# Optimization experiments

Measured on AMD Instinct MI355X. Metric: run time of the kernel, lower is better.

## Reference

```python
import jax, jax.numpy as jnp
import numpy as np

N_NODES = 10000
N_EDGES = 160000
N_FEAT = 128      # n_features
N_BASIS = 20      # n_basis
N_LAYERS = 3      # n_interactions
N_GRAPHS = 64
CUTOFF = 5.0
VOCAB = 119       # 118 elements + padding idx 0


def setup_inputs() -> dict:
    key = jax.random.key(0)
    ks = jax.random.split(key, 20)
    z = jax.random.randint(ks[0], (N_NODES,), 0, VOCAB)
    pos = jax.random.normal(ks[1], (N_NODES, 3), dtype=jnp.float32) * 2.0
    cell = jax.random.normal(ks[2], (N_GRAPHS, 3, 3), dtype=jnp.float32)
    batch = jnp.sort(jax.random.randint(ks[3], (N_NODES,), 0, N_GRAPHS))
    edge_index = jax.random.randint(ks[4], (2, N_EDGES), 0, N_NODES)

    s = 1.0 / np.sqrt(N_FEAT)
    node_emb = jax.random.normal(ks[5], (VOCAB, N_FEAT), dtype=jnp.float32) * 0.1
    node_emb = node_emb.at[0].set(0.0)  # padding_idx=0
    # per-layer stacked parameters (L, ...)
    mnp_W1 = jax.random.normal(ks[6], (N_LAYERS, N_FEAT, N_FEAT), dtype=jnp.float32) * s
    mnp_b1 = jnp.zeros((N_LAYERS, N_FEAT), dtype=jnp.float32)
    mnp_W2 = jax.random.normal(ks[7], (N_LAYERS, N_FEAT, N_FEAT), dtype=jnp.float32) * s
    mnp_b2 = jnp.zeros((N_LAYERS, N_FEAT), dtype=jnp.float32)
    me_W = jax.random.normal(ks[8], (N_LAYERS, N_BASIS, N_FEAT), dtype=jnp.float32) * (1.0 / np.sqrt(N_BASIS))
    em1_W1 = jax.random.normal(ks[9], (N_LAYERS, N_FEAT, N_FEAT), dtype=jnp.float32) * s
    em1_W2 = jax.random.normal(ks[10], (N_LAYERS, N_FEAT, N_FEAT), dtype=jnp.float32) * s
    em2_W1 = jax.random.normal(ks[11], (N_LAYERS, N_FEAT, N_FEAT), dtype=jnp.float32) * s
    em2_W2 = jax.random.normal(ks[12], (N_LAYERS, N_FEAT, N_FEAT), dtype=jnp.float32) * s
    eu_W = jax.random.normal(ks[13], (N_LAYERS, N_FEAT, N_FEAT), dtype=jnp.float32) * s
    return {
        "z": z, "pos": pos, "cell": cell, "batch": batch, "edge_index": edge_index,
        "node_emb": node_emb,
        "mnp_W1": mnp_W1, "mnp_b1": mnp_b1, "mnp_W2": mnp_W2, "mnp_b2": mnp_b2,
        "me_W": me_W, "em1_W1": em1_W1, "em1_W2": em1_W2,
        "em2_W1": em2_W1, "em2_W2": em2_W2, "eu_W": eu_W,
    }


def _edge_embedding(pos_d, edge_index):
    """Gaussian RBF x cosine cutoff; dir = unit displacement vectors."""
    i, j = edge_index[0], edge_index[1]
    diff = pos_d[j] - pos_d[i]                      # (E, 3)
    d = jnp.sqrt(jnp.sum(diff * diff, axis=-1) + 1e-12)  # (E,)
    dir_edge = diff / d[:, None]                    # (E, 3)
    centers = jnp.linspace(0.0, CUTOFF, N_BASIS)
    width = CUTOFF / N_BASIS
    rbf = jnp.exp(-jnp.square((d[:, None] - centers) / width))  # (E, B)
    fc = 0.5 * (jnp.cos(jnp.pi * d / CUTOFF) + 1.0) * (d < CUTOFF)
    return rbf * fc[:, None], dir_edge


def reference(z, pos, cell, batch, edge_index, node_emb,
              mnp_W1, mnp_b1, mnp_W2, mnp_b2, me_W,
              em1_W1, em1_W2, em2_W1, em2_W2, eu_W):
    n = z.shape[0]
    atom = node_emb[z]                                   # (N, F)
    force = jnp.zeros((n, 3, N_FEAT), dtype=pos.dtype)   # (N, 3, F)

    # strain displacement bookkeeping (identity in plain forward)
    disp = jnp.broadcast_to(jnp.eye(3, dtype=pos.dtype), cell.shape)  # (G,3,3)
    sym = 0.5 * (disp + jnp.swapaxes(disp, -1, -2))
    pos_d = jnp.einsum('nd,nde->ne', pos, sym[batch])

    dist_edge, dir_edge = _edge_embedding(pos_d, edge_index)
    i, j = edge_index[0], edge_index[1]

    for l in range(N_LAYERS):
        # invariant node/edge message parts
        h = jax.nn.silu(atom @ mnp_W1[l] + mnp_b1[l]) @ mnp_W2[l] + mnp_b2[l]  # (N,F)
        me = dist_edge @ me_W[l]                                               # (E,F)
        msg = me * h[i] * h[j]                                                 # (E,F)
        atom = atom + jax.ops.segment_sum(msg, i, num_segments=n)
        # equivariant messages
        e1 = (jax.nn.silu(msg @ em1_W1[l]) @ em1_W2[l])[:, None, :] * dir_edge[:, :, None]  # (E,3,F)
        e2 = (jax.nn.silu(msg @ em2_W1[l]) @ em2_W2[l])[:, None, :] * force[j]              # (E,3,F)
        force = force + jax.ops.segment_sum(e1 + e2, i, num_segments=n)
        atom = atom + jnp.sum(force * (force @ eu_W[l]), axis=1)
    return atom, force
```

## Files before the change

### kernel.cpp

```cpp
#include <hip/hip_runtime.h>
#include <hip/hip_bf16.h>
#include <math.h>

#define NN 10000
#define NE 160000
#define NF 128
#define NB 20
#define CUT 5.0f
#define TPS 136
#define TPF 132

typedef __attribute__((ext_vector_type(8))) short short8;
typedef __attribute__((ext_vector_type(4))) float floatx4;
typedef unsigned short u16;
typedef unsigned int u32;

__device__ __forceinline__ u16 f2b(float x){
  union { __hip_bfloat16 b; u16 u; } cv;
  cv.b = __float2bfloat16(x);
  return cv.u;
}
__device__ __forceinline__ float lo_bf(u32 w){ return __uint_as_float(w << 16); }
__device__ __forceinline__ float hi_bf(u32 w){ return __uint_as_float(w & 0xFFFF0000u); }
__device__ __forceinline__ float fast_silu(float v){
  return v * __builtin_amdgcn_rcpf(1.f + __expf(-v));
}
__device__ __forceinline__ float rdf(const void* p, size_t i, int isb){
  return isb ? __bfloat162float(((const __hip_bfloat16*)p)[i]) : ((const float*)p)[i];
}

__global__ __launch_bounds__(256) void k_detect(const void* __restrict__ w, int nelem,
                                                int* __restrict__ flag){
  __shared__ int cnt;
  if (threadIdx.x == 0) cnt = 0;
  __syncthreads();
  const u16* hw = (const u16*)w;
  int local = 0;
  for (int k = threadIdx.x; k < nelem; k += 256){
    u16 h = hw[k];
    int e = (h >> 7) & 0xFF;
    if ((h & 0x7FFF) == 0 || (e >= 103 && e <= 130)) local++;
  }
  atomicAdd(&cnt, local);
  __syncthreads();
  if (threadIdx.x == 0) *flag = (cnt >= (nelem * 9) / 10) ? 1 : 0;
}

struct PrepArgs {
  const void* csrc[4]; float* cdst[4]; int cn[4];
  const void* ssrc[7]; u16* sdst[7];
  const void* mesrc;   u16* medst;
};
__global__ __launch_bounds__(256) void k_prep(PrepArgs a, const int* __restrict__ flag){
  int y = blockIdx.y;
  int isb = *flag;
  if (y < 4){
    const void* s = a.csrc[y]; float* d = a.cdst[y]; int n = a.cn[y];
    for (int i = blockIdx.x*256 + threadIdx.x; i < n; i += gridDim.x*256)
      d[i] = rdf(s, i, isb);
  } else if (y < 11){
    const void* s = a.ssrc[y-4]; u16* d = a.sdst[y-4];
    int idx = blockIdx.x*256 + threadIdx.x;
    int l = idx >> 14, rem = idx & 16383;
    int j = rem & 7, lane = (rem >> 3) & 63, tn = (rem >> 9) & 7, tk = rem >> 12;
    int k = tk*32 + ((lane >> 4) & 3)*8 + j, n = tn*16 + (lane & 15);
    d[idx] = f2b(rdf(s, (size_t)l*16384 + k*NF + n, isb));
  } else {
    int idx = blockIdx.x*256 + threadIdx.x;
    if (idx >= 3*4096) return;
    int l = idx >> 12, rem = idx & 4095;
    int j = rem & 7, lane = (rem >> 3) & 63, tn = rem >> 9;
    int k = ((lane >> 4) & 3)*8 + j, n = tn*16 + (lane & 15);
    a.medst[idx] = (k < NB) ? f2b(rdf(a.mesrc, (size_t)l*NB*NF + k*NF + n, isb)) : (u16)0;
  }
}

__global__ __launch_bounds__(256) void k_hist(const int* __restrict__ ei, int* __restrict__ count){
  int e = blockIdx.x*256 + threadIdx.x;
  if (e < NE) atomicAdd(&count[ei[e]], 1);
}
__global__ __launch_bounds__(256) void k_scan(const int* __restrict__ count,
                                              int* __restrict__ rowptr, int* __restrict__ cursor){
  __shared__ int part[256];
  const int CH = (NN + 255) / 256;
  int t = threadIdx.x;
  int base = t * CH;
  int s = 0;
  for (int k = 0; k < CH; k++){ int i = base + k; if (i < NN) s += count[i]; }
  part[t] = s;
  __syncthreads();
  for (int off = 1; off < 256; off <<= 1){
    int v = (t >= off) ? part[t - off] : 0;
    __syncthreads();
    part[t] += v;
    __syncthreads();
  }
  int run = (t == 0) ? 0 : part[t - 1];
  for (int k = 0; k < CH; k++){
    int i = base + k;
    if (i < NN){ rowptr[i] = run; cursor[i] = run; run += count[i]; }
  }
  if (t == 255) rowptr[NN] = run;
}
__global__ __launch_bounds__(256) void k_scatter_embed(const int* __restrict__ ei,
                                                       int* __restrict__ cursor,
                                                       const float* __restrict__ pos,
                                                       int* __restrict__ iis, int* __restrict__ jjs,
                                                       float* __restrict__ ds,
                                                       float* __restrict__ dirs){
  int e = blockIdx.x * 256 + threadIdx.x;
  if (e >= NE) return;
  int i = ei[e], j = ei[NE + e];
  float dx = pos[j*3+0] - pos[i*3+0];
  float dy = pos[j*3+1] - pos[i*3+1];
  float dz = pos[j*3+2] - pos[i*3+2];
  float d = sqrtf(dx*dx + dy*dy + dz*dz + 1e-12f);
  float inv = 1.0f / d;
  int s = atomicAdd(&cursor[i], 1);
  iis[s] = i; jjs[s] = j;
  ds[s] = d;
  dirs[s*3+0] = dx*inv; dirs[s*3+1] = dy*inv; dirs[s*3+2] = dz*inv;
}
__global__ __launch_bounds__(256) void k_rbf(const float* __restrict__ ds,
                                             u16* __restrict__ rbfb){
  int e = blockIdx.x * 256 + threadIdx.x;
  if (e >= NE) return;
  float d = ds[e];
  float fc = (d < CUT) ? 0.5f*(cosf((float)M_PI*d*(1.0f/CUT)) + 1.0f) : 0.0f;
  u32 row[16];
  #pragma unroll
  for (int kk = 0; kk < 16; kk++){
    int k0 = kk*2, k1 = kk*2 + 1;
    u32 w = 0;
    if (k0 < NB){
      float t0 = (d - CUT*(float)k0/(float)(NB-1)) * ((float)NB/CUT);
      w = (u32)f2b(__expf(-t0*t0) * fc);
    }
    if (k1 < NB){
      float t1 = (d - CUT*(float)k1/(float)(NB-1)) * ((float)NB/CUT);
      w |= ((u32)f2b(__expf(-t1*t1) * fc)) << 16;
    }
    row[kk] = w;
  }
  float4* dst = (float4*)(rbfb + (size_t)e*32);
  #pragma unroll
  for (int jv = 0; jv < 4; jv++)
    dst[jv] = *(const float4*)&row[jv*4];
}

__global__ __launch_bounds__(128, 2) void k_mlp0(
    const int* __restrict__ z, const float* __restrict__ emb,
    float* __restrict__ atom,
    const u16* __restrict__ w1sw, const float* __restrict__ b1,
    const u16* __restrict__ w2sw, const float* __restrict__ b2,
    u32* __restrict__ hb)
{
  __shared__ __align__(16) u16 tileT[16][TPS];
  const int wv = threadIdx.x >> 6;
  const int lane = threadIdx.x & 63;
  const int q = lane >> 4, ln = lane & 15;
  const int n0 = blockIdx.x * 16;
  const int zn = z[n0 + ln];

  floatx4 c1[4];
  #pragma unroll
  for (int t = 0; t < 4; t++) c1[t] = (floatx4){0,0,0,0};
  #pragma unroll
  for (int tk = 0; tk < 4; tk++){
    const float4 u0 = *(const float4*)&emb[(size_t)zn*NF + tk*32 + q*8];
    const float4 u1 = *(const float4*)&emb[(size_t)zn*NF + tk*32 + q*8 + 4];
    if ((tk >> 1) == wv){
      *(float4*)&atom[(size_t)(n0+ln)*NF + tk*32 + q*8]     = u0;
      *(float4*)&atom[(size_t)(n0+ln)*NF + tk*32 + q*8 + 4] = u1;
    }
    short8 a;
    a[0]=(short)f2b(u0.x); a[1]=(short)f2b(u0.y); a[2]=(short)f2b(u0.z); a[3]=(short)f2b(u0.w);
    a[4]=(short)f2b(u1.x); a[5]=(short)f2b(u1.y); a[6]=(short)f2b(u1.z); a[7]=(short)f2b(u1.w);
    #pragma unroll
    for (int t = 0; t < 4; t++){
      short8 b = *(const short8*)(w1sw + (size_t)((tk*8 + wv*4 + t)*64 + lane)*8);
      c1[t] = __builtin_amdgcn_mfma_f32_16x16x32_bf16(a, b, c1[t], 0, 0, 0);
    }
  }
  #pragma unroll
  for (int t = 0; t < 4; t++){
    int n = (wv*4 + t)*16 + ln;
    float bias = b1[n];
    #pragma unroll
    for (int r = 0; r < 4; r++)
      tileT[q*4 + r][n] = f2b(fast_silu(c1[t][r] + bias));
  }
  __syncthreads();
  floatx4 c2[4];
  #pragma unroll
  for (int t = 0; t < 4; t++) c2[t] = (floatx4){0,0,0,0};
  #pragma unroll
  for (int tk = 0; tk < 4; tk++){
    short8 a = *(const short8*)&tileT[ln][tk*32 + q*8];
    #pragma unroll
    for (int t = 0; t < 4; t++){
      short8 b = *(const short8*)(w2sw + (size_t)((tk*8 + wv*4 + t)*64 + lane)*8);
      c2[t] = __builtin_amdgcn_mfma_f32_16x16x32_bf16(a, b, c2[t], 0, 0, 0);
    }
  }
  #pragma unroll
  for (int t = 0; t < 4; t++){
    float bias = b2[(wv*4 + t)*16 + ln];
    #pragma unroll
    for (int r = 0; r < 4; r++)
      ((u16*)hb)[(((size_t)(n0 + q*4 + r))*64 + t*16 + ln)*2 + wv] = f2b(c2[t][r] + bias);
  }
}

#define SEGFLUSH(ADDR_EXPR)                                               \
  {                                                                       \
    float s_ = 0.f;                                                       \
    _Pragma("unroll")                                                     \
    for (int m_ = 0; m_ < 16; m_++){                                      \
      s_ += tileF[m_][cc];                                                \
      if (m_ == 15 || ((bmask >> (m_ + 1)) & 1u)){                        \
        int ii_ = __builtin_amdgcn_readlane(curii, m_);                   \
        float* p_ = (ADDR_EXPR);                                          \
        atomicAdd(p_ + cc, s_);                                           \
        s_ = 0.f;                                                         \
      }                                                                   \
    }                                                                     \
  }

__global__ __launch_bounds__(128, 4) void k_edge_mfma(
    const int* __restrict__ iis, const int* __restrict__ jjs,
    const u16* __restrict__ rbfb, const float* __restrict__ dirs,
    const u32* __restrict__ hb,
    const u16* __restrict__ mesw,
    const u16* __restrict__ w11sw, const u16* __restrict__ w12sw,
    const u16* __restrict__ w21sw, const u16* __restrict__ w22sw,
    float* __restrict__ atom, const u32* __restrict__ forceb, float* __restrict__ force)
{
  __shared__ __align__(16) u16 tileM[16][TPS];
  __shared__ __align__(16) float tileF[16][TPF];
  u16* tileFu = (u16*)&tileF[0][0];

  const int wv = threadIdx.x >> 6;
  const int lane = threadIdx.x & 63;
  const int q = lane >> 4, ln = lane & 15;
  const int bid = (blockIdx.x & 7) * (gridDim.x >> 3) + (blockIdx.x >> 3);
  const int e0 = bid * 16;
  const int cc = wv*64 + lane;

  const int l16 = lane & 15;
  int curii = iis[e0 + l16];
  int previi = (l16 == 0) ? ~curii : iis[e0 + l16 - 1];
  const u32 bmask = (u32)__ballot(lane < 16 && (curii != previi));

  int iiR[4], jjR[4];
  float dirR[4][3];
  #pragma unroll
  for (int r = 0; r < 4; r++){
    int s = e0 + q*4 + r;
    iiR[r] = iis[s]; jjR[r] = jjs[s];
    dirR[r][0] = dirs[s*3+0]; dirR[r][1] = dirs[s*3+1]; dirR[r][2] = dirs[s*3+2];
  }

  u32 hiw[4][4], hjw[4][4];
  #pragma unroll
  for (int r = 0; r < 4; r++)
    #pragma unroll
    for (int t = 0; t < 4; t++){
      hiw[r][t] = hb[(size_t)iiR[r]*64 + t*16 + ln];
      hjw[r][t] = hb[(size_t)jjR[r]*64 + t*16 + ln];
    }

  short8 a_rbf = *(const short8*)(rbfb + (size_t)(e0 + ln)*32 + q*8);

  #pragma unroll
  for (int t = 0; t < 4; t++){
    const int tn_g = wv*4 + t;
    short8 b = *(const short8*)(mesw + (size_t)(tn_g*64 + lane)*8);
    floatx4 c = {0.f,0.f,0.f,0.f};
    c = __builtin_amdgcn_mfma_f32_16x16x32_bf16(a_rbf, b, c, 0, 0, 0);
    const int n = tn_g*16 + ln;
    #pragma unroll
    for (int r = 0; r < 4; r++){
      float hi_ = wv ? hi_bf(hiw[r][t]) : lo_bf(hiw[r][t]);
      float hj_ = wv ? hi_bf(hjw[r][t]) : lo_bf(hjw[r][t]);
      float mv = c[r] * hi_ * hj_;
      tileF[q*4 + r][n] = mv;
      tileM[q*4 + r][n] = f2b(mv);
    }
  }

  SEGFLUSH(&atom[(size_t)ii_ * NF])

  __syncthreads();

  floatx4 c2[4], c1[4];
  #pragma unroll
  for (int t = 0; t < 4; t++){ c2[t] = (floatx4){0,0,0,0}; c1[t] = (floatx4){0,0,0,0}; }
  #pragma unroll
  for (int tk = 0; tk < 4; tk++){
    short8 a = *(const short8*)&tileM[ln][tk*32 + q*8];
    #pragma unroll
    for (int t = 0; t < 4; t++){
      const int tn_g = wv*4 + t;
      short8 b2 = *(const short8*)(w21sw + (size_t)((tk*8 + tn_g)*64 + lane)*8);
      c2[t] = __builtin_amdgcn_mfma_f32_16x16x32_bf16(a, b2, c2[t], 0, 0, 0);
      short8 b1 = *(const short8*)(w11sw + (size_t)((tk*8 + tn_g)*64 + lane)*8);
      c1[t] = __builtin_amdgcn_mfma_f32_16x16x32_bf16(a, b1, c1[t], 0, 0, 0);
    }
  }
  #pragma unroll
  for (int t = 0; t < 4; t++){
    const int n = (wv*4 + t)*16 + ln;
    #pragma unroll
    for (int r = 0; r < 4; r++){
      tileFu[(q*4 + r)*TPS + n] = f2b(fast_silu(c1[t][r]));
      c2[t][r] = fast_silu(c2[t][r]);
    }
  }

  __syncthreads();

  floatx4 g1[4];
  #pragma unroll
  for (int t = 0; t < 4; t++) g1[t] = (floatx4){0,0,0,0};
  #pragma unroll
  for (int tk = 0; tk < 4; tk++){
    short8 a = *(const short8*)&tileFu[(size_t)ln*TPS + tk*32 + q*8];
    #pragma unroll
    for (int t = 0; t < 4; t++){
      short8 b = *(const short8*)(w12sw + (size_t)((tk*8 + wv*4 + t)*64 + lane)*8);
      g1[t] = __builtin_amdgcn_mfma_f32_16x16x32_bf16(a, b, g1[t], 0, 0, 0);
    }
  }
  #pragma unroll
  for (int t = 0; t < 4; t++){
    const int n = (wv*4 + t)*16 + ln;
    #pragma unroll
    for (int r = 0; r < 4; r++) tileM[q*4 + r][n] = f2b(c2[t][r]);
  }

  __syncthreads();

  floatx4 g2[4];
  #pragma unroll
  for (int t = 0; t < 4; t++) g2[t] = (floatx4){0,0,0,0};
  #pragma unroll
  for (int tk = 0; tk < 4; tk++){
    short8 a = *(const short8*)&tileM[ln][tk*32 + q*8];
    #pragma unroll
    for (int t = 0; t < 4; t++){
      short8 b = *(const short8*)(w22sw + (size_t)((tk*8 + wv*4 + t)*64 + lane)*8);
      g2[t] = __builtin_amdgcn_mfma_f32_16x16x32_bf16(a, b, g2[t], 0, 0, 0);
    }
  }

  for (int d = 0; d < 3; d++){
    u32 fjw[4][4];
    #pragma unroll
    for (int r = 0; r < 4; r++)
      #pragma unroll
      for (int t = 0; t < 4; t++)
        fjw[r][t] = forceb[((size_t)jjR[r]*3 + d)*64 + t*16 + ln];
    #pragma unroll
    for (int t = 0; t < 4; t++){
      const int n = (wv*4 + t)*16 + ln;
      #pragma unroll
      for (int r = 0; r < 4; r++){
        float fj = wv ? hi_bf(fjw[r][t]) : lo_bf(fjw[r][t]);
        tileF[q*4 + r][n] = g1[t][r]*dirR[r][d] + g2[t][r]*fj;
      }
    }
    SEGFLUSH(&force[((size_t)ii_*3 + d)*NF])
  }
}

__global__ __launch_bounds__(256, 2) void k_node(
    const float* __restrict__ force,
    const u16* __restrict__ eusw, u32* __restrict__ forceb,
    float* __restrict__ atom,
    const u16* __restrict__ w1sw, const float* __restrict__ b1,
    const u16* __restrict__ w2sw, const float* __restrict__ b2,
    u32* __restrict__ hb, int do_mlp)
{
  __shared__ __align__(16) u16 tileM3[3][16][TPS];
  __shared__ __align__(16) float tileF3[3][16][TPF];
  const int w = threadIdx.x >> 6;
  const int lane = threadIdx.x & 63;
  const int q = lane >> 4, ln = lane & 15;
  const int n0 = blockIdx.x * 16;
  const int cc2 = threadIdx.x & 127;
  const int mh  = (threadIdx.x >> 7) * 8;

  #pragma unroll
  for (int d = 0; d < 3; d++)
    #pragma unroll
    for (int m8 = 0; m8 < 8; m8++){
      int m = mh + m8;
      size_t idx = ((size_t)(n0+m)*3 + d)*NF + cc2;
      float v = force[idx];
      if (do_mlp)
        ((u16*)forceb)[(((size_t)(n0+m)*3 + d)*64 + (cc2 & 63))*2 + (cc2 >> 6)] = f2b(v);
      tileM3[d][m][cc2] = f2b(v);
      tileF3[d][m][cc2] = v;
    }
  __syncthreads();

  float acc[2][4];
  #pragma unroll
  for (int t = 0; t < 2; t++)
    #pragma unroll
    for (int r = 0; r < 4; r++) acc[t][r] = 0.f;

  #pragma unroll
  for (int d = 0; d < 3; d++){
    floatx4 c[2];
    #pragma unroll
    for (int t = 0; t < 2; t++) c[t] = (floatx4){0,0,0,0};
    #pragma unroll
    for (int tk = 0; tk < 4; tk++){
      short8 a = *(const short8*)&tileM3[d][ln][tk*32 + q*8];
      #pragma unroll
      for (int t = 0; t < 2; t++){
        short8 b = *(const short8*)(eusw + (size_t)((tk*8 + w*2 + t)*64 + lane)*8);
        c[t] = __builtin_amdgcn_mfma_f32_16x16x32_bf16(a, b, c[t], 0, 0, 0);
      }
    }
    #pragma unroll
    for (int t = 0; t < 2; t++){
      int n = (w*2 + t)*16 + ln;
      #pragma unroll
      for (int r = 0; r < 4; r++)
        acc[t][r] += tileF3[d][q*4 + r][n] * c[t][r];
    }
  }

  float anew[2][4];
  #pragma unroll
  for (int t = 0; t < 2; t++){
    int n = (w*2 + t)*16 + ln;
    #pragma unroll
    for (int r = 0; r < 4; r++){
      size_t idx = (size_t)(n0 + q*4 + r)*NF + n;
      float v = atom[idx] + acc[t][r];
      atom[idx] = v;
      anew[t][r] = v;
    }
  }
  if (!do_mlp) return;

  u16 (*tile)[TPS] = tileM3[0];
  __syncthreads();
  #pragma unroll
  for (int t = 0; t < 2; t++){
    int n = (w*2 + t)*16 + ln;
    #pragma unroll
    for (int r = 0; r < 4; r++) tile[q*4 + r][n] = f2b(anew[t][r]);
  }
  __syncthreads();
  floatx4 c1[2];
  #pragma unroll
  for (int t = 0; t < 2; t++) c1[t] = (floatx4){0,0,0,0};
  #pragma unroll
  for (int tk = 0; tk < 4; tk++){
    short8 a = *(const short8*)&tile[ln][tk*32 + q*8];
    #pragma unroll
    for (int t = 0; t < 2; t++){
      short8 b = *(const short8*)(w1sw + (size_t)((tk*8 + w*2 + t)*64 + lane)*8);
      c1[t] = __builtin_amdgcn_mfma_f32_16x16x32_bf16(a, b, c1[t], 0, 0, 0);
    }
  }
  __syncthreads();
  #pragma unroll
  for (int t = 0; t < 2; t++){
    int n = (w*2 + t)*16 + ln;
    float bias = b1[n];
    #pragma unroll
    for (int r = 0; r < 4; r++)
      tile[q*4 + r][n] = f2b(fast_silu(c1[t][r] + bias));
  }
  __syncthreads();
  floatx4 c2[2];
  #pragma unroll
  for (int t = 0; t < 2; t++) c2[t] = (floatx4){0,0,0,0};
  #pragma unroll
  for (int tk = 0; tk < 4; tk++){
    short8 a = *(const short8*)&tile[ln][tk*32 + q*8];
    #pragma unroll
    for (int t = 0; t < 2; t++){
      short8 b = *(const short8*)(w2sw + (size_t)((tk*8 + w*2 + t)*64 + lane)*8);
      c2[t] = __builtin_amdgcn_mfma_f32_16x16x32_bf16(a, b, c2[t], 0, 0, 0);
    }
  }
  #pragma unroll
  for (int t = 0; t < 2; t++){
    int tn = w*2 + t;
    float bias = b2[tn*16 + ln];
    #pragma unroll
    for (int r = 0; r < 4; r++)
      ((u16*)hb)[(((size_t)(n0 + q*4 + r))*64 + (tn & 3)*16 + ln)*2 + (tn >> 2)] = f2b(c2[t][r] + bias);
  }
}

__global__ __launch_bounds__(256) void k_writeout(const float* __restrict__ atom,
                                                  const float* __restrict__ force,
                                                  void* __restrict__ out,
                                                  const int* __restrict__ flag){
  int idx = blockIdx.x * 256 + threadIdx.x;
  const int na = NN * NF;
  const int tot = na + NN * 3 * NF;
  if (idx >= tot) return;
  float v = (idx < na) ? atom[idx] : force[idx - na];
  if (*flag) ((__hip_bfloat16*)out)[idx] = __float2bfloat16(v);
  else       ((float*)out)[idx] = v;
}

extern "C" void kernel_launch(void* const* d_in, const int* in_sizes, int n_in,
                              void* d_out, int out_size, void* d_ws, size_t ws_size,
                              hipStream_t stream){
  const int* z    = (const int*)d_in[0];
  const void* pos = d_in[1];
  const int* ei   = (const int*)d_in[4];
  const void* emb   = d_in[5];
  const void* mnpW1 = d_in[6];
  const void* mnpb1 = d_in[7];
  const void* mnpW2 = d_in[8];
  const void* mnpb2 = d_in[9];
  const void* meW   = d_in[10];
  const void* em1W1 = d_in[11];
  const void* em1W2 = d_in[12];
  const void* em2W1 = d_in[13];
  const void* em2W2 = d_in[14];
  const void* euW   = d_in[15];

  float* base  = (float*)d_ws;
  int*   flag  = (int*)d_ws;
  float* atom   = base + 4;
  float* force  = atom   + NN*NF;
  u32*   forceb = (u32*)(force + (size_t)NN*3*NF);
  int*   count  = (int*)(forceb + (size_t)NN*3*64);
  float* ds    = (float*)(count + NN);
  float* dirs  = ds + NE;
  float* posf  = dirs + 3*NE;
  float* embf  = posf + NN*3;
  float* b1f   = embf + 119*NF;
  float* b2f_  = b1f + 3*NF;
  u32*   hb    = (u32*)(b2f_ + 3*NF);
  u16*   mesw  = (u16*)(hb + (size_t)NN*64);
  u16*   w11sw = mesw  + 3*4096;
  u16*   w12sw = w11sw + 3*16384;
  u16*   w21sw = w12sw + 3*16384;
  u16*   w22sw = w21sw + 3*16384;
  u16*   w1sw  = w22sw + 3*16384;
  u16*   w2sw  = w1sw  + 3*16384;
  u16*   eusw  = w2sw  + 3*16384;
  int* rowptr  = (int*)(eusw + 3*16384);
  int* cursor  = rowptr + NN + 1;
  int* iis     = cursor + NN;
  int* jjs     = iis + NE;
  u16* rbfb    = (u16*)(jjs + NE);

  k_detect<<<1, 256, 0, stream>>>(meW, 3*NB*NF, flag);

  hipMemsetAsync(force, 0, ((size_t)NN*3*NF + (size_t)NN*3*64 + NN)*4, stream);

  PrepArgs pa;
  pa.csrc[0]=pos;   pa.cdst[0]=posf; pa.cn[0]=NN*3;
  pa.csrc[1]=emb;   pa.cdst[1]=embf; pa.cn[1]=119*NF;
  pa.csrc[2]=mnpb1; pa.cdst[2]=b1f;  pa.cn[2]=3*NF;
  pa.csrc[3]=mnpb2; pa.cdst[3]=b2f_; pa.cn[3]=3*NF;
  pa.ssrc[0]=em1W1; pa.sdst[0]=w11sw;
  pa.ssrc[1]=em1W2; pa.sdst[1]=w12sw;
  pa.ssrc[2]=em2W1; pa.sdst[2]=w21sw;
  pa.ssrc[3]=em2W2; pa.sdst[3]=w22sw;
  pa.ssrc[4]=mnpW1; pa.sdst[4]=w1sw;
  pa.ssrc[5]=mnpW2; pa.sdst[5]=w2sw;
  pa.ssrc[6]=euW;   pa.sdst[6]=eusw;
  pa.mesrc=meW;     pa.medst=mesw;
  k_prep<<<dim3(192,12), 256, 0, stream>>>(pa, flag);

  k_hist         <<<(NE+255)/256, 256, 0, stream>>>(ei, count);
  k_scan         <<<1, 256, 0, stream>>>(count, rowptr, cursor);
  k_scatter_embed<<<(NE+255)/256, 256, 0, stream>>>(ei, cursor, posf, iis, jjs, ds, dirs);
  k_rbf          <<<(NE+255)/256, 256, 0, stream>>>(ds, rbfb);

  k_mlp0<<<NN/16, 128, 0, stream>>>(z, embf, atom, w1sw, b1f, w2sw, b2f_, hb);
  for (int l = 0; l < 3; l++){
    k_edge_mfma<<<NE/16, 128, 0, stream>>>(iis, jjs, rbfb, dirs, hb,
        mesw  + (size_t)l*4096,
        w11sw + (size_t)l*16384, w12sw + (size_t)l*16384,
        w21sw + (size_t)l*16384, w22sw + (size_t)l*16384,
        atom, forceb, force);
    int nl = l + 1;
    k_node<<<NN/16, 256, 0, stream>>>(force,
        eusw + (size_t)l*16384, forceb, atom,
        w1sw + (size_t)(nl%3)*16384, b1f + (size_t)(nl%3)*NF,
        w2sw + (size_t)(nl%3)*16384, b2f_ + (size_t)(nl%3)*NF,
        hb, (l < 2) ? 1 : 0);
  }

  k_writeout<<<(NN*NF + NN*3*NF + 255)/256, 256, 0, stream>>>(atom, force, d_out, flag);
}
```

Measured before the change: 484.3 us.

## Split edge kernel column tiles across four waves per block

The edge kernel now launches 256 threads per block, so each of four waves handles two 16-column output tiles instead of four. Accumulator and gathered-feature register arrays shrink, and the segmented atomic flush is restricted to the lower 32 lanes so 128 columns map onto 256 threads. This aims to raise wave-level parallelism and latency hiding for the gathers and MFMA chains. In exchange it adds per-wave redundant A-tile LDS reads and idle lanes during the atomic flushes.

```diff
diff --git a/kernel.cpp b/kernel.cpp
--- a/kernel.cpp
+++ b/kernel.cpp
@@ -227,7 +227,7 @@
     }                                                                     \
   }
 
-__global__ __launch_bounds__(128, 4) void k_edge_mfma(
+__global__ __launch_bounds__(256, 2) void k_edge_mfma(
     const int* __restrict__ iis, const int* __restrict__ jjs,
     const u16* __restrict__ rbfb, const float* __restrict__ dirs,
     const u32* __restrict__ hb,
@@ -240,12 +240,14 @@
   __shared__ __align__(16) float tileF[16][TPF];
   u16* tileFu = (u16*)&tileF[0][0];
 
-  const int wv = threadIdx.x >> 6;
+  const int w = threadIdx.x >> 6;
   const int lane = threadIdx.x & 63;
   const int q = lane >> 4, ln = lane & 15;
+  const int half = w >> 1;
+  const int wt = (w & 1) * 2;
   const int bid = (blockIdx.x & 7) * (gridDim.x >> 3) + (blockIdx.x >> 3);
   const int e0 = bid * 16;
-  const int cc = wv*64 + lane;
+  const int cc = w*32 + (lane & 31);
 
   const int l16 = lane & 15;
   int curii = iis[e0 + l16];
@@ -261,47 +263,49 @@
     dirR[r][0] = dirs[s*3+0]; dirR[r][1] = dirs[s*3+1]; dirR[r][2] = dirs[s*3+2];
   }
 
-  u32 hiw[4][4], hjw[4][4];
+  u32 hiw[4][2], hjw[4][2];
   #pragma unroll
   for (int r = 0; r < 4; r++)
     #pragma unroll
-    for (int t = 0; t < 4; t++){
-      hiw[r][t] = hb[(size_t)iiR[r]*64 + t*16 + ln];
-      hjw[r][t] = hb[(size_t)jjR[r]*64 + t*16 + ln];
+    for (int t = 0; t < 2; t++){
+      hiw[r][t] = hb[(size_t)iiR[r]*64 + (wt + t)*16 + ln];
+      hjw[r][t] = hb[(size_t)jjR[r]*64 + (wt + t)*16 + ln];
     }
 
   short8 a_rbf = *(const short8*)(rbfb + (size_t)(e0 + ln)*32 + q*8);
 
   #pragma unroll
-  for (int t = 0; t < 4; t++){
-    const int tn_g = wv*4 + t;
+  for (int t = 0; t < 2; t++){
+    const int tn_g = w*2 + t;
     short8 b = *(const short8*)(mesw + (size_t)(tn_g*64 + lane)*8);
     floatx4 c = {0.f,0.f,0.f,0.f};
     c = __builtin_amdgcn_mfma_f32_16x16x32_bf16(a_rbf, b, c, 0, 0, 0);
     const int n = tn_g*16 + ln;
     #pragma unroll
     for (int r = 0; r < 4; r++){
-      float hi_ = wv ? hi_bf(hiw[r][t]) : lo_bf(hiw[r][t]);
-      float hj_ = wv ? hi_bf(hjw[r][t]) : lo_bf(hjw[r][t]);
+      float hi_ = half ? hi_bf(hiw[r][t]) : lo_bf(hiw[r][t]);
+      float hj_ = half ? hi_bf(hjw[r][t]) : lo_bf(hjw[r][t]);
       float mv = c[r] * hi_ * hj_;
       tileF[q*4 + r][n] = mv;
       tileM[q*4 + r][n] = f2b(mv);
     }
   }
 
-  SEGFLUSH(&atom[(size_t)ii_ * NF])
-
-  __syncthreads();
-
-  floatx4 c2[4], c1[4];
-  #pragma unroll
-  for (int t = 0; t < 4; t++){ c2[t] = (floatx4){0,0,0,0}; c1[t] = (floatx4){0,0,0,0}; }
+  if (lane < 32){
+    SEGFLUSH(&atom[(size_t)ii_ * NF])
+  }
+
+  __syncthreads();
+
+  floatx4 c2[2], c1[2];
+  #pragma unroll
+  for (int t = 0; t < 2; t++){ c2[t] = (floatx4){0,0,0,0}; c1[t] = (floatx4){0,0,0,0}; }
   #pragma unroll
   for (int tk = 0; tk < 4; tk++){
     short8 a = *(const short8*)&tileM[ln][tk*32 + q*8];
     #pragma unroll
-    for (int t = 0; t < 4; t++){
-      const int tn_g = wv*4 + t;
+    for (int t = 0; t < 2; t++){
+      const int tn_g = w*2 + t;
       short8 b2 = *(const short8*)(w21sw + (size_t)((tk*8 + tn_g)*64 + lane)*8);
       c2[t] = __builtin_amdgcn_mfma_f32_16x16x32_bf16(a, b2, c2[t], 0, 0, 0);
       short8 b1 = *(const short8*)(w11sw + (size_t)((tk*8 + tn_g)*64 + lane)*8);
@@ -309,8 +313,8 @@
     }
   }
   #pragma unroll
-  for (int t = 0; t < 4; t++){
-    const int n = (wv*4 + t)*16 + ln;
+  for (int t = 0; t < 2; t++){
+    const int n = (w*2 + t)*16 + ln;
     #pragma unroll
     for (int r = 0; r < 4; r++){
       tileFu[(q*4 + r)*TPS + n] = f2b(fast_silu(c1[t][r]));
@@ -320,57 +324,59 @@
 
   __syncthreads();
 
-  floatx4 g1[4];
-  #pragma unroll
-  for (int t = 0; t < 4; t++) g1[t] = (floatx4){0,0,0,0};
+  floatx4 g1[2];
+  #pragma unroll
+  for (int t = 0; t < 2; t++) g1[t] = (floatx4){0,0,0,0};
   #pragma unroll
   for (int tk = 0; tk < 4; tk++){
     short8 a = *(const short8*)&tileFu[(size_t)ln*TPS + tk*32 + q*8];
     #pragma unroll
-    for (int t = 0; t < 4; t++){
-      short8 b = *(const short8*)(w12sw + (size_t)((tk*8 + wv*4 + t)*64 + lane)*8);
+    for (int t = 0; t < 2; t++){
+      short8 b = *(const short8*)(w12sw + (size_t)((tk*8 + w*2 + t)*64 + lane)*8);
       g1[t] = __builtin_amdgcn_mfma_f32_16x16x32_bf16(a, b, g1[t], 0, 0, 0);
     }
   }
   #pragma unroll
-  for (int t = 0; t < 4; t++){
-    const int n = (wv*4 + t)*16 + ln;
+  for (int t = 0; t < 2; t++){
+    const int n = (w*2 + t)*16 + ln;
     #pragma unroll
     for (int r = 0; r < 4; r++) tileM[q*4 + r][n] = f2b(c2[t][r]);
   }
 
   __syncthreads();
 
-  floatx4 g2[4];
-  #pragma unroll
-  for (int t = 0; t < 4; t++) g2[t] = (floatx4){0,0,0,0};
+  floatx4 g2[2];
+  #pragma unroll
+  for (int t = 0; t < 2; t++) g2[t] = (floatx4){0,0,0,0};
   #pragma unroll
   for (int tk = 0; tk < 4; tk++){
     short8 a = *(const short8*)&tileM[ln][tk*32 + q*8];
     #pragma unroll
-    for (int t = 0; t < 4; t++){
-      short8 b = *(const short8*)(w22sw + (size_t)((tk*8 + wv*4 + t)*64 + lane)*8);
+    for (int t = 0; t < 2; t++){
+      short8 b = *(const short8*)(w22sw + (size_t)((tk*8 + w*2 + t)*64 + lane)*8);
       g2[t] = __builtin_amdgcn_mfma_f32_16x16x32_bf16(a, b, g2[t], 0, 0, 0);
     }
   }
 
   for (int d = 0; d < 3; d++){
-    u32 fjw[4][4];
+    u32 fjw[4][2];
     #pragma unroll
     for (int r = 0; r < 4; r++)
       #pragma unroll
-      for (int t = 0; t < 4; t++)
-        fjw[r][t] = forceb[((size_t)jjR[r]*3 + d)*64 + t*16 + ln];
-    #pragma unroll
-    for (int t = 0; t < 4; t++){
-      const int n = (wv*4 + t)*16 + ln;
+      for (int t = 0; t < 2; t++)
+        fjw[r][t] = forceb[((size_t)jjR[r]*3 + d)*64 + (wt + t)*16 + ln];
+    #pragma unroll
+    for (int t = 0; t < 2; t++){
+      const int n = (w*2 + t)*16 + ln;
       #pragma unroll
       for (int r = 0; r < 4; r++){
-        float fj = wv ? hi_bf(fjw[r][t]) : lo_bf(fjw[r][t]);
+        float fj = half ? hi_bf(fjw[r][t]) : lo_bf(fjw[r][t]);
         tileF[q*4 + r][n] = g1[t][r]*dirR[r][d] + g2[t][r]*fj;
       }
     }
-    SEGFLUSH(&force[((size_t)ii_*3 + d)*NF])
+    if (lane < 32){
+      SEGFLUSH(&force[((size_t)ii_*3 + d)*NF])
+    }
   }
 }
 
@@ -585,7 +591,7 @@
 
   k_mlp0<<<NN/16, 128, 0, stream>>>(z, embf, atom, w1sw, b1f, w2sw, b2f_, hb);
   for (int l = 0; l < 3; l++){
-    k_edge_mfma<<<NE/16, 128, 0, stream>>>(iis, jjs, rbfb, dirs, hb,
+    k_edge_mfma<<<NE/16, 256, 0, stream>>>(iis, jjs, rbfb, dirs, hb,
         mesw  + (size_t)l*4096,
         w11sw + (size_t)l*16384, w12sw + (size_t)l*16384,
         w21sw + (size_t)l*16384, w22sw + (size_t)l*16384,
```

Result: slower. 504.9 us (+4.3%).
